# Kernel optimization log

Hardware: AMD Instinct MI355X
Metric: run time of the kernel (lower is better)

Reference implementation:

```python
import jax, jax.numpy as jnp
import numpy as np

B, NB, NV, H = 512, 3, 64, 256
CS = (40, 40)          # child branch lengths
COUP = (16, 48)        # parent vertices where child branches attach
IN = 9


def setup_inputs() -> dict:
    key = jax.random.key(0)
    ks = jax.random.split(key, 24)

    def w(k, shape, fan_in):
        return jax.random.uniform(k, shape, jnp.float32, -1.0, 1.0) / np.sqrt(fan_in)

    return {
        "current_vertices": jax.random.normal(ks[0], (B, NB, NV, 3), jnp.float32),
        "previous_vertices": jax.random.normal(ks[1], (B, NB, NV, 3), jnp.float32),
        "clamped_target_hints": jax.random.normal(ks[2], (B, NB, NV, 3), jnp.float32),
        # encoder
        "enc_w1": w(ks[3], (IN, H), IN), "enc_b1": w(ks[4], (H,), IN),
        "enc_w2": w(ks[5], (H, H), H), "enc_b2": w(ks[6], (H,), H),
        # child-sum tree-LSTM cell (bottom-up)
        "W_iou": w(ks[7], (H, 3 * H), H), "b_iou": w(ks[8], (3 * H,), H),
        "U_iou": w(ks[9], (H, 3 * H), H),
        "W_f": w(ks[10], (H, H), H), "b_f": w(ks[11], (H,), H),
        "U_f": w(ks[12], (H, H), H),
        # torch.nn.LSTMCell (top-down), gate order i,f,g,o
        "W_ih": w(ks[13], (H, 4 * H), H), "b_ih": w(ks[14], (4 * H,), H),
        "W_hh": w(ks[15], (H, 4 * H), H), "b_hh": w(ks[16], (4 * H,), H),
        # decoder
        "dec_w1": w(ks[17], (2 * H, H), 2 * H), "dec_b1": w(ks[18], (H,), 2 * H),
        "dec_w2": w(ks[19], (H, 3), H), "dec_b2": w(ks[20], (3,), H),
    }


def _forward(cv, pv, hints,
             enc_w1, enc_b1, enc_w2, enc_b2,
             W_iou, b_iou, U_iou, W_f, b_f, U_f,
             W_ih, b_ih, W_hh, b_hh,
             dec_w1, dec_b1, dec_w2, dec_b2):
    Bsz = cv.shape[0]
    nv = cv.shape[2]
    dt = cv.dtype
    feats = jnp.concatenate([cv, cv - pv, hints], axis=-1)            # [B,NB,NV,9]
    enc = jnp.maximum(feats @ enc_w1 + enc_b1, 0.0) @ enc_w2 + enc_b2  # [B,NB,NV,H]
    zero = jnp.zeros((Bsz, H), dt)

    # --- bottom-up: child-sum cell. A leaf with a single all-zero child is
    # mathematically identical to a zero initial carry (U_* have no bias),
    # so each chain is a plain scan from leaf toward vertex 0.
    def bu_chain_step(carry, x):
        h_prev, c_prev = carry
        iou = x @ W_iou + b_iou + h_prev @ U_iou
        i, o, u = jnp.split(iou, 3, axis=-1)
        f = jax.nn.sigmoid(x @ W_f + b_f + h_prev @ U_f)
        c = jax.nn.sigmoid(i) * jnp.tanh(u) + f * c_prev
        h = jax.nn.sigmoid(o) * jnp.tanh(c)
        return (h, c), (h, c)

    # child branches: leaf (v=L-1) -> v=0
    roots_h, roots_c, child_bu = [], [], []
    for k, L in enumerate(CS):
        xs = jnp.transpose(enc[:, k + 1, :L], (1, 0, 2))[::-1]  # time-major, reversed
        _, (hs, cs) = jax.lax.scan(bu_chain_step, (zero, zero), xs)
        hs, cs = hs[::-1], cs[::-1]                              # [L,B,H] indexed by v
        roots_h.append(hs[0]); roots_c.append(cs[0])
        child_bu.append((hs, cs))

    # coupled-child states injected at coupling vertices of the parent chain
    K = len(CS)
    coup_h = jnp.zeros((nv, K, Bsz, H), dt)
    coup_c = jnp.zeros_like(coup_h)
    coup_m = jnp.zeros((nv, K), dt)
    for k, ci in enumerate(COUP):
        coup_h = coup_h.at[ci, k].set(roots_h[k])
        coup_c = coup_c.at[ci, k].set(roots_c[k])
        coup_m = coup_m.at[ci, k].set(1.0)

    def bu_parent_step(carry, inp):
        h_prev, c_prev = carry
        x, ch, cc, m = inp  # ch,cc: [K,B,H]; m: [K]
        h_sum = h_prev + (m[:, None, None] * ch).sum(0)
        iou = x @ W_iou + b_iou + h_sum @ U_iou
        i, o, u = jnp.split(iou, 3, axis=-1)
        wf = x @ W_f + b_f
        fc = jax.nn.sigmoid(wf + h_prev @ U_f) * c_prev
        fc = fc + (m[:, None, None] * jax.nn.sigmoid(wf[None] + ch @ U_f) * cc).sum(0)
        c = jax.nn.sigmoid(i) * jnp.tanh(u) + fc
        h = jax.nn.sigmoid(o) * jnp.tanh(c)
        return (h, c), (h, c)

    xs0 = jnp.transpose(enc[:, 0], (1, 0, 2))  # [NV,B,H]
    _, (p_hs, p_cs) = jax.lax.scan(
        bu_parent_step, (zero, zero),
        (xs0[::-1], coup_h[::-1], coup_c[::-1], coup_m[::-1]))
    p_hs, p_cs = p_hs[::-1], p_cs[::-1]

    bu_h = jnp.zeros((Bsz, NB, nv, H), dt)
    bu_c = jnp.zeros_like(bu_h)
    bu_h = bu_h.at[:, 0].set(jnp.transpose(p_hs, (1, 0, 2)))
    bu_c = bu_c.at[:, 0].set(jnp.transpose(p_cs, (1, 0, 2)))
    for k, L in enumerate(CS):
        hs, cs = child_bu[k]
        bu_h = bu_h.at[:, k + 1, :L].set(jnp.transpose(hs, (1, 0, 2)))
        bu_c = bu_c.at[:, k + 1, :L].set(jnp.transpose(cs, (1, 0, 2)))

    # --- top-down: standard LSTMCell chains
    def td_step(carry, x):
        h, c = carry
        g = x @ W_ih + b_ih + h @ W_hh + b_hh
        i, f, gg, o = jnp.split(g, 4, axis=-1)
        c = jax.nn.sigmoid(f) * c + jax.nn.sigmoid(i) * jnp.tanh(gg)
        h = jax.nn.sigmoid(o) * jnp.tanh(c)
        return (h, c), (h, c)

    _, (t_hs, t_cs) = jax.lax.scan(td_step, (bu_h[:, 0, 0], bu_c[:, 0, 0]), xs0[1:])
    td_p_h = jnp.concatenate([bu_h[:, 0, 0][None], t_hs], 0)  # [NV,B,H]
    td_p_c = jnp.concatenate([bu_c[:, 0, 0][None], t_cs], 0)

    td_h = jnp.zeros_like(bu_h)
    td_h = td_h.at[:, 0].set(jnp.transpose(td_p_h, (1, 0, 2)))
    for k, L in enumerate(CS):
        xs = jnp.transpose(enc[:, k + 1, :L], (1, 0, 2))
        _, (hs, _) = jax.lax.scan(td_step, (td_p_h[COUP[k]], td_p_c[COUP[k]]), xs)
        td_h = td_h.at[:, k + 1, :L].set(jnp.transpose(hs, (1, 0, 2)))

    comb = jnp.concatenate([bu_h, td_h], axis=-1)  # [B,NB,NV,2H]
    delta = jnp.maximum(comb @ dec_w1 + dec_b1, 0.0) @ dec_w2 + dec_b2
    pred = cv + delta
    mask = jnp.ones((NB, nv, 1), dt)
    for k, L in enumerate(CS):
        mask = mask.at[k + 1, L:].set(0.0)
    return pred * mask[None]


def reference(current_vertices, previous_vertices, clamped_target_hints,
              enc_w1, enc_b1, enc_w2, enc_b2,
              W_iou, b_iou, U_iou, W_f, b_f, U_f,
              W_ih, b_ih, W_hh, b_hh,
              dec_w1, dec_b1, dec_w2, dec_b2):
    return _forward(current_vertices, previous_vertices, clamped_target_hints,
                    enc_w1, enc_b1, enc_w2, enc_b2,
                    W_iou, b_iou, U_iou, W_f, b_f, U_f,
                    W_ih, b_ih, W_hh, b_hh,
                    dec_w1, dec_b1, dec_w2, dec_b2)
```

## Files before the change

kernel.cpp:

```cpp
#include <hip/hip_runtime.h>
#include <hip/hip_bf16.h>
#include <hip/hip_fp8.h>


constexpr int Hd    = 256;
constexpr int NBv   = 3;
constexpr int NVv   = 64;
constexpr int BATCH = 512;
constexpr long long NROWS = (long long)BATCH * NBv * NVv;
constexpr int CLEN = 40;
constexpr int CI0 = 16, CI1 = 48;

typedef __hip_bfloat16 bf16;
typedef unsigned short ushort;
typedef unsigned char u8;
typedef __attribute__((ext_vector_type(8))) short short8;
typedef __attribute__((ext_vector_type(4))) float f32x4;
typedef __attribute__((ext_vector_type(2))) long longx2;

__device__ __forceinline__ float sigf(float x)   { return 1.f / (1.f + __expf(-x)); }
__device__ __forceinline__ float tanh_f(float x) { return 1.f - 2.f / (__expf(2.f * x) + 1.f); }

__device__ __forceinline__ ushort f2bf(float x) {
  unsigned u = __float_as_uint(x);
  return (ushort)((u + 0x7FFFu + ((u >> 16) & 1u)) >> 16);
}
__device__ __forceinline__ float bf2f(ushort u) {
  return __uint_as_float(((unsigned)u) << 16);
}
__device__ __forceinline__ u8 f2fp8(float x) {
  __hip_fp8_e4m3 q(x);
  return (u8)q.__x;
}


__global__ __launch_bounds__(256) void pack_bu8_kernel(
    const float* __restrict__ W_iou, const float* __restrict__ W_f,
    const float* __restrict__ U_iou, const float* __restrict__ U_f,
    u8* __restrict__ out)
{
  int u = blockIdx.x * 256 + threadIdx.x;
  int s = u & 1, l = (u >> 1) & 63, T = u >> 7;
  int kp = T & 7, nt = T >> 3;
  int ks = kp * 2 + s;
  int k0 = ks * 32 + (l >> 4) * 8;
  int n  = nt * 16 + (l & 15);
  unsigned long long r = 0;
#pragma unroll
  for (int j = 0; j < 8; ++j) {
    int k = k0 + j;
    float v;
    if (k < 256) v = (n < 768) ? W_iou[k * 768 + n] : W_f[k * 256 + (n - 768)];
    else         v = (n < 768) ? U_iou[(k - 256) * 768 + n] : U_f[(k - 256) * 256 + (n - 768)];
    r |= ((unsigned long long)f2fp8(v)) << (8 * j);
  }
  *(unsigned long long*)(out + (size_t)u * 8) = r;
}

__global__ __launch_bounds__(256) void pack_td8_kernel(
    const float* __restrict__ W_ih, const float* __restrict__ W_hh,
    u8* __restrict__ out)
{
  int u = blockIdx.x * 256 + threadIdx.x;
  int s = u & 1, l = (u >> 1) & 63, T = u >> 7;
  int kp = T & 7, nt = T >> 3;
  int ks = kp * 2 + s;
  int k0 = ks * 32 + (l >> 4) * 8;
  int n  = nt * 16 + (l & 15);
  unsigned long long r = 0;
#pragma unroll
  for (int j = 0; j < 8; ++j) {
    int k = k0 + j;
    float v = (k < 256) ? W_ih[k * 1024 + n] : W_hh[(k - 256) * 1024 + n];
    r |= ((unsigned long long)f2fp8(v)) << (8 * j);
  }
  *(unsigned long long*)(out + (size_t)u * 8) = r;
}

__global__ __launch_bounds__(256) void pack_wfx8_kernel(
    const float* __restrict__ W_f, u8* __restrict__ out)
{
  int u = blockIdx.x * 256 + threadIdx.x;
  int s = u & 1, l = (u >> 1) & 63, T = u >> 7;
  int kp = T & 3, nt = T >> 2;
  int ks = kp * 2 + s;
  int k0 = ks * 32 + (l >> 4) * 8;
  int n  = nt * 16 + (l & 15);
  unsigned long long r = 0;
#pragma unroll
  for (int j = 0; j < 8; ++j)
    r |= ((unsigned long long)f2fp8(W_f[(k0 + j) * 256 + n])) << (8 * j);
  *(unsigned long long*)(out + (size_t)u * 8) = r;
}

__global__ __launch_bounds__(256) void pack_encw2_kernel(
    const float* __restrict__ w2, ushort* __restrict__ out)
{
  int idx = blockIdx.x * 256 + threadIdx.x;
  int j = idx & 7, l = (idx >> 3) & 63, T = idx >> 9;
  int ks = T & 7, nt = T >> 3;
  int k = ks * 32 + (l >> 4) * 8 + j;
  int n = nt * 16 + (l & 15);
  out[idx] = f2bf(w2[k * 256 + n]);
}

__global__ __launch_bounds__(256) void pack_decw1_kernel(
    const float* __restrict__ w1, ushort* __restrict__ out)
{
  int idx = blockIdx.x * 256 + threadIdx.x;
  int j = idx & 7, l = (idx >> 3) & 63, T = idx >> 9;
  int ks = T & 15, nt = T >> 4;
  int k = ks * 32 + (l >> 4) * 8 + j;
  int n = nt * 16 + (l & 15);
  out[idx] = f2bf(w1[k * 256 + n]);
}

__global__ __launch_bounds__(256) void pack_decw2_kernel(
    const float* __restrict__ w2, ushort* __restrict__ out)
{
  int idx = blockIdx.x * 256 + threadIdx.x;
  int j = idx & 7, l = (idx >> 3) & 63, T = idx >> 9;
  int ks = T & 7;
  int k = ks * 32 + (l >> 4) * 8 + j;
  int n = l & 15;
  out[idx] = (n < 3) ? f2bf(w2[k * 3 + n]) : (ushort)0;
}

__device__ __forceinline__ short8 ldA16(const ushort* buf, int row, int kbyte) {
  int off = (row * 512 + kbyte) ^ ((row & 7) << 4);
  return *(const short8*)((const char*)buf + off);
}
__device__ __forceinline__ short8 ldA1024(const ushort* buf, int row, int kbyte) {
  int off = (row * 1024 + kbyte) ^ ((row & 7) << 4);
  return *(const short8*)((const char*)buf + off);
}
#define STA(BUF, R, JJ, BITS) { \
    int off_ = ((R) * 512 + (JJ) * 2) ^ (((R) & 7) << 4); \
    (BUF)[off_ >> 1] = (BITS); }
#define STA8(BUF, R, JJ, B8) { \
    int off_ = ((R) * 256 + (JJ)) ^ (((R) & 7) << 3); \
    (BUF)[off_] = (B8); }

__global__ __launch_bounds__(256) void enc_kernel(
    const float* __restrict__ cv, const float* __restrict__ pv,
    const float* __restrict__ hints,
    const float* __restrict__ w1, const float* __restrict__ b1,
    const ushort* __restrict__ w2p, const float* __restrict__ b2,
    ushort* __restrict__ enc)
{
  __shared__ float fs[32][10];
  __shared__ ushort h1L[32 * 256];
  const long long row0 = (long long)blockIdx.x * 32;
  const int tid = threadIdx.x;
  if (tid < 96) {
    int r = tid / 3, c = tid % 3;
    long long row = row0 + r;
    float a = cv[row * 3 + c];
    fs[r][c]     = a;
    fs[r][3 + c] = a - pv[row * 3 + c];
    fs[r][6 + c] = hints[row * 3 + c];
  }
  __syncthreads();
  {
    const int j = tid;
    float wc[9];
#pragma unroll
    for (int i = 0; i < 9; ++i) wc[i] = w1[i * 256 + j];
    const float bb = b1[j];
    for (int r = 0; r < 32; ++r) {
      float a = bb;
#pragma unroll
      for (int i = 0; i < 9; ++i) a += fs[r][i] * wc[i];
      ushort hb = f2bf(fmaxf(a, 0.f));
      STA(h1L, r, j, hb);
    }
  }
  __syncthreads();
  const int lane = tid & 63, w = tid >> 6;
  const int col = lane & 15, krow = lane >> 4, kb = krow * 16;
  const f32x4 zf4 = {0.f, 0.f, 0.f, 0.f};
  f32x4 acc[2][4];
#pragma unroll
  for (int m = 0; m < 2; ++m)
#pragma unroll
    for (int g = 0; g < 4; ++g) acc[m][g] = zf4;
#pragma unroll
  for (int ks = 0; ks < 8; ++ks) {
    short8 A[2];
#pragma unroll
    for (int m = 0; m < 2; ++m) A[m] = ldA16(h1L, m * 16 + col, ks * 64 + kb);
#pragma unroll
    for (int g = 0; g < 4; ++g) {
      short8 b = *(const short8*)(w2p + ((((w * 4 + g) * 8 + ks) * 64 + lane)) * 8);
#pragma unroll
      for (int m = 0; m < 2; ++m)
        acc[m][g] = __builtin_amdgcn_mfma_f32_16x16x32_bf16(A[m], b, acc[m][g], 0, 0, 0);
    }
  }
#pragma unroll
  for (int g = 0; g < 4; ++g) {
    const int jj = (w * 4 + g) * 16 + col;
    const float bb = b2[jj];
#pragma unroll
    for (int m = 0; m < 2; ++m)
#pragma unroll
      for (int q = 0; q < 4; ++q) {
        long long row = row0 + m * 16 + krow * 4 + q;
        enc[row * 256 + jj] = f2bf(acc[m][g][q] + bb);
      }
  }
}

template<int MT>
__device__ __forceinline__ void gemm_main8(
    const u8* __restrict__ W, const u8* __restrict__ AxL,
    const u8* __restrict__ AhL, f32x4 (&acc)[MT][4], int w, int lane)
{
  const int col = lane & 15;
  const int kb  = (lane >> 4) * 8;
  const int sw  = (col & 7) << 3;
#pragma unroll 4
  for (int kp = 0; kp < 8; ++kp) {
    const u8* Ab = (kp < 4) ? AxL : AhL;
    const int ksl = (kp & 3) * 2;
    long a[MT][2];
#pragma unroll
    for (int m = 0; m < MT; ++m) {
      int base = (m * 16 + col) * 256 + ksl * 32 + kb;
      a[m][0] = *(const long*)(Ab + ((base) ^ sw));
      a[m][1] = *(const long*)(Ab + ((base + 32) ^ sw));
    }
#pragma unroll
    for (int g = 0; g < 4; ++g) {
      longx2 bq = *(const longx2*)(W + ((size_t)(((g * 16 + w) * 8 + kp) * 64 + lane) << 4));
#pragma unroll
      for (int m = 0; m < MT; ++m) {
        acc[m][g] = __builtin_amdgcn_mfma_f32_16x16x32_fp8_fp8(a[m][0], bq[0], acc[m][g], 0, 0, 0);
        acc[m][g] = __builtin_amdgcn_mfma_f32_16x16x32_fp8_fp8(a[m][1], bq[1], acc[m][g], 0, 0, 0);
      }
    }
  }
}

__device__ __forceinline__ void gemm_side8(
    const u8* __restrict__ Wbu, const u8* __restrict__ Wfx,
    const u8* __restrict__ Rhb, const u8* __restrict__ AxL,
    f32x4 (&accs)[4], f32x4& accw, int w, int lane)
{
  const int col = lane & 15;
  const int kb  = (lane >> 4) * 8;
  const int sw  = (col & 7) << 3;
#pragma unroll
  for (int kp = 0; kp < 4; ++kp) {
    const int base = col * 256 + kp * 64 + kb;
    long ar0 = *(const long*)(Rhb + ((base) ^ sw));
    long ar1 = *(const long*)(Rhb + ((base + 32) ^ sw));
#pragma unroll
    for (int g = 0; g < 4; ++g) {
      longx2 bq = *(const longx2*)(Wbu + ((size_t)(((g * 16 + w) * 8 + kp + 4) * 64 + lane) << 4));
      accs[g] = __builtin_amdgcn_mfma_f32_16x16x32_fp8_fp8(ar0, bq[0], accs[g], 0, 0, 0);
      accs[g] = __builtin_amdgcn_mfma_f32_16x16x32_fp8_fp8(ar1, bq[1], accs[g], 0, 0, 0);
    }
    long ax0 = *(const long*)(AxL + ((base) ^ sw));
    long ax1 = *(const long*)(AxL + ((base + 32) ^ sw));
    longx2 bw = *(const longx2*)(Wfx + ((size_t)((w * 4 + kp) * 64 + lane) << 4));
    accw = __builtin_amdgcn_mfma_f32_16x16x32_fp8_fp8(ax0, bw[0], accw, 0, 0, 0);
    accw = __builtin_amdgcn_mfma_f32_16x16x32_fp8_fp8(ax1, bw[1], accw, 0, 0, 0);
  }
}

#define ZACC(MT_, A_) { \
  _Pragma("unroll") for (int m_ = 0; m_ < MT_; ++m_) \
  _Pragma("unroll") for (int g_ = 0; g_ < 4; ++g_) A_[m_][g_] = zf4; }

__global__ __launch_bounds__(1024, 4) void seq_kernel(
    const ushort* enc,
    const u8* __restrict__ Wbu, const u8* __restrict__ Wtd,
    const u8* __restrict__ Wfx,
    const float* __restrict__ b_iou, const float* __restrict__ b_f,
    const float* __restrict__ b_ih,  const float* __restrict__ b_hh,
    ushort* __restrict__ bu_h, ushort* td_h)
{
  __shared__ u8 Axb[2][32 * 256];
  __shared__ u8 Ahb[2][32 * 256];
  __shared__ u8 Rh[2][16 * 256];

  const int tid  = threadIdx.x;
  const int lane = tid & 63;
  const int w    = tid >> 6;
  const int b0   = blockIdx.x * 16;
  const int col  = lane & 15;
  const int krow = lane >> 4;
  const f32x4 zf4 = {0.f, 0.f, 0.f, 0.f};

  const int jj = w * 16 + col;
  const float bi0 = b_iou[jj], bi1 = b_iou[256 + jj], bi2 = b_iou[512 + jj];
  const float bfv = b_f[jj];
  const float bt0 = b_ih[jj]       + b_hh[jj];
  const float bt1 = b_ih[256 + jj] + b_hh[256 + jj];
  const float bt2 = b_ih[512 + jj] + b_hh[512 + jj];
  const float bt3 = b_ih[768 + jj] + b_hh[768 + jj];

  float c2[2][4];
  float rc0[4], rc1[4];
  float sc0[4], sc1[4];

#define SLOAD32(V, XV) { \
    int rr_ = tid >> 5, ch_ = tid & 31; \
    int mt_ = rr_ >> 4, br_ = rr_ & 15; \
    long long rowg_ = ((long long)(b0 + br_) * NBv + (mt_ + 1)) * NVv + (V); \
    XV = *(const short8*)(enc + rowg_ * 256 + ch_ * 8); }

#define SLOAD16(V, XV) if (tid < 512) { \
    int rr_ = tid >> 5, ch_ = tid & 31; \
    long long rowg_ = ((long long)(b0 + rr_) * NBv) * NVv + (V); \
    XV = *(const short8*)(enc + rowg_ * 256 + ch_ * 8); }

#define SWRITE(DST, XV, GUARD) if (GUARD) { \
    int rr_ = tid >> 5, ch_ = tid & 31; \
    unsigned long long r_ = 0; \
    _Pragma("unroll") for (int e_ = 0; e_ < 8; ++e_) \
      r_ |= ((unsigned long long)f2fp8(bf2f((ushort)XV[e_]))) << (8 * e_); \
    *(unsigned long long*)((DST) + (((rr_ * 256 + ch_ * 8) ^ ((rr_ & 7) << 3)))) = r_; }

  {
    *(unsigned long long*)(&Ahb[0][tid * 8]) = 0ull;
    short8 xv; SLOAD32(CLEN - 1, xv);
#pragma unroll
    for (int m = 0; m < 2; ++m)
#pragma unroll
      for (int q = 0; q < 4; ++q) c2[m][q] = 0.f;
    SWRITE(Axb[0], xv, true);
    __syncthreads();
    for (int s = 0; s < CLEN; ++s) {
      const int v = CLEN - 1 - s, pp = s & 1;
      short8 xn;
      if (s < CLEN - 1) SLOAD32(v - 1, xn);
      f32x4 acc[2][4]; ZACC(2, acc);
      gemm_main8<2>(Wbu, Axb[pp], Ahb[pp], acc, w, lane);
#pragma unroll
      for (int m = 0; m < 2; ++m)
#pragma unroll
        for (int q = 0; q < 4; ++q) {
          const int br = krow * 4 + q;
          float I = acc[m][0][q] + bi0;
          float O = acc[m][1][q] + bi1;
          float U = acc[m][2][q] + bi2;
          float F = acc[m][3][q] + bfv;
          float cn = sigf(I) * tanh_f(U) + sigf(F) * c2[m][q];
          float hn = sigf(O) * tanh_f(cn);
          c2[m][q] = cn;
          u8 hq = f2fp8(hn);
          STA8(Ahb[pp ^ 1], m * 16 + br, jj, hq);
          long long rowg = ((long long)(b0 + br) * NBv + (m + 1)) * NVv + v;
          bu_h[rowg * 256 + jj] = f2bf(hn);
          if (v == 0) {
            STA8(Rh[m], br, jj, hq);
            if (m == 0) rc0[q] = cn; else rc1[q] = cn;
          }
        }
      if (s < CLEN - 1) SWRITE(Axb[pp ^ 1], xn, true);
      __syncthreads();
    }
  }

  {
    if (tid < 512) *(unsigned long long*)(&Ahb[0][tid * 8]) = 0ull;
    short8 xv = {};
    SLOAD16(NVv - 1, xv);
#pragma unroll
    for (int q = 0; q < 4; ++q) c2[0][q] = 0.f;
    SWRITE(Axb[0], xv, (tid < 512));
    __syncthreads();
    for (int s = 0; s < NVv; ++s) {
      const int v = NVv - 1 - s, pp = s & 1;
      short8 xn = {};
      if (s < NVv - 1) SLOAD16(v - 1, xn);
      f32x4 acc[1][4]; ZACC(1, acc);
      gemm_main8<1>(Wbu, Axb[pp], Ahb[pp], acc, w, lane);
      const int ck = (v == CI0) ? 0 : ((v == CI1) ? 1 : -1);
      f32x4 accs[4]; f32x4 accw;
      if (ck >= 0) {
#pragma unroll
        for (int g = 0; g < 4; ++g) accs[g] = zf4;
        accw = zf4;
        const u8* Rp = (ck == 0) ? Rh[0] : Rh[1];
        gemm_side8(Wbu, Wfx, Rp, Axb[pp], accs, accw, w, lane);
      }
#pragma unroll
      for (int q = 0; q < 4; ++q) {
        const int br = krow * 4 + q;
        float I  = acc[0][0][q] + bi0;
        float O  = acc[0][1][q] + bi1;
        float U  = acc[0][2][q] + bi2;
        float F1 = acc[0][3][q] + bfv;
        float fc = sigf(F1) * c2[0][q];
        if (ck >= 0) {
          I += accs[0][q]; O += accs[1][q]; U += accs[2][q];
          float wfx = accw[q] + bfv;
          float rcv = (ck == 0) ? rc0[q] : rc1[q];
          fc += sigf(wfx + accs[3][q]) * rcv;
        }
        float cn = sigf(I) * tanh_f(U) + fc;
        float hn = sigf(O) * tanh_f(cn);
        c2[0][q] = cn;
        STA8(Ahb[pp ^ 1], br, jj, f2fp8(hn));
        long long rowg = ((long long)(b0 + br) * NBv) * NVv + v;
        bu_h[rowg * 256 + jj] = f2bf(hn);
        if (v == 0) td_h[rowg * 256 + jj] = f2bf(hn);
      }
      if (s < NVv - 1) SWRITE(Axb[pp ^ 1], xn, (tid < 512));
      __syncthreads();
    }
  }

  {
    short8 xv = {};
    SLOAD16(1, xv);
    SWRITE(Axb[0], xv, (tid < 512));
    __syncthreads();
    for (int s = 0; s < NVv - 1; ++s) {
      const int v = 1 + s, pp = s & 1;
      short8 xn = {};
      if (s < NVv - 2) SLOAD16(v + 1, xn);
      f32x4 acc[1][4]; ZACC(1, acc);
      gemm_main8<1>(Wtd, Axb[pp], Ahb[pp], acc, w, lane);
#pragma unroll
      for (int q = 0; q < 4; ++q) {
        const int br = krow * 4 + q;
        float I = acc[0][0][q] + bt0;
        float F = acc[0][1][q] + bt1;
        float G = acc[0][2][q] + bt2;
        float O = acc[0][3][q] + bt3;
        float cn = sigf(F) * c2[0][q] + sigf(I) * tanh_f(G);
        float hn = sigf(O) * tanh_f(cn);
        c2[0][q] = cn;
        u8 hq = f2fp8(hn);
        STA8(Ahb[pp ^ 1], br, jj, hq);
        long long rowg = ((long long)(b0 + br) * NBv) * NVv + v;
        td_h[rowg * 256 + jj] = f2bf(hn);
        if (v == CI0) { STA8(Rh[0], br, jj, hq); sc0[q] = cn; }
        if (v == CI1) { STA8(Rh[1], br, jj, hq); sc1[q] = cn; }
      }
      if (s < NVv - 2) SWRITE(Axb[pp ^ 1], xn, (tid < 512));
      __syncthreads();
    }
  }

  {
    {
      int rr = tid >> 5, ch = tid & 31;
      int mt = rr >> 4, br = rr & 15;
      unsigned long long vv = *(const unsigned long long*)(
          &Rh[mt][0] + (((br * 256 + ch * 8) ^ ((br & 7) << 3))));
      *(unsigned long long*)(&Ahb[0][0] + (((rr * 256 + ch * 8) ^ ((rr & 7) << 3)))) = vv;
    }
    short8 xv; SLOAD32(0, xv);
#pragma unroll
    for (int m = 0; m < 2; ++m)
#pragma unroll
      for (int q = 0; q < 4; ++q)
        c2[m][q] = (m == 0) ? sc0[q] : sc1[q];
    SWRITE(Axb[0], xv, true);
    __syncthreads();
    for (int s = 0; s < CLEN; ++s) {
      const int v = s, pp = s & 1;
      short8 xn;
      if (s < CLEN - 1) SLOAD32(v + 1, xn);
      f32x4 acc[2][4]; ZACC(2, acc);
      gemm_main8<2>(Wtd, Axb[pp], Ahb[pp], acc, w, lane);
#pragma unroll
      for (int m = 0; m < 2; ++m)
#pragma unroll
        for (int q = 0; q < 4; ++q) {
          const int br = krow * 4 + q;
          float I = acc[m][0][q] + bt0;
          float F = acc[m][1][q] + bt1;
          float G = acc[m][2][q] + bt2;
          float O = acc[m][3][q] + bt3;
          float cn = sigf(F) * c2[m][q] + sigf(I) * tanh_f(G);
          float hn = sigf(O) * tanh_f(cn);
          c2[m][q] = cn;
          STA8(Ahb[pp ^ 1], m * 16 + br, jj, f2fp8(hn));
          long long rowg = ((long long)(b0 + br) * NBv + (m + 1)) * NVv + v;
          td_h[rowg * 256 + jj] = f2bf(hn);
        }
      if (s < CLEN - 1) SWRITE(Axb[pp ^ 1], xn, true);
      __syncthreads();
    }
  }
}

__global__ __launch_bounds__(256) void dec_kernel(
    const ushort* __restrict__ bu_h, const ushort* __restrict__ td_h,
    const float* __restrict__ cv,
    const ushort* __restrict__ w1p, const float* __restrict__ b1,
    const ushort* __restrict__ w2p, const float* __restrict__ b2,
    float* __restrict__ out)
{
  __shared__ ushort combL[32 * 512];
  __shared__ ushort hidL[32 * 256];
  const long long row0 = (long long)blockIdx.x * 32;
  const int tid = threadIdx.x;

#pragma unroll
  for (int h = 0; h < 8; ++h) {
    int cid = tid + h * 256;
    int rr = cid >> 6, ch = cid & 63;
    long long row = row0 + rr;
    short8 v = (ch < 32)
        ? *(const short8*)(bu_h + row * 256 + ch * 8)
        : *(const short8*)(td_h + row * 256 + (ch - 32) * 8);
    *(short8*)((char*)combL + ((rr * 1024 + ch * 16) ^ ((rr & 7) << 4))) = v;
  }
  __syncthreads();

  const int lane = tid & 63, w = tid >> 6;
  const int col = lane & 15, krow = lane >> 4, kb = krow * 16;
  const f32x4 zf4 = {0.f, 0.f, 0.f, 0.f};
  f32x4 acc[2][4];
#pragma unroll
  for (int m = 0; m < 2; ++m)
#pragma unroll
    for (int g = 0; g < 4; ++g) acc[m][g] = zf4;
#pragma unroll 4
  for (int ks = 0; ks < 16; ++ks) {
    short8 A[2];
#pragma unroll
    for (int m = 0; m < 2; ++m) A[m] = ldA1024(combL, m * 16 + col, ks * 64 + kb);
#pragma unroll
    for (int g = 0; g < 4; ++g) {
      short8 b = *(const short8*)(w1p + ((((w * 4 + g) * 16 + ks) * 64 + lane)) * 8);
#pragma unroll
      for (int m = 0; m < 2; ++m)
        acc[m][g] = __builtin_amdgcn_mfma_f32_16x16x32_bf16(A[m], b, acc[m][g], 0, 0, 0);
    }
  }
#pragma unroll
  for (int g = 0; g < 4; ++g) {
    const int jj = (w * 4 + g) * 16 + col;
    const float bb = b1[jj];
#pragma unroll
    for (int m = 0; m < 2; ++m)
#pragma unroll
      for (int q = 0; q < 4; ++q) {
        ushort hb = f2bf(fmaxf(acc[m][g][q] + bb, 0.f));
        STA(hidL, m * 16 + krow * 4 + q, jj, hb);
      }
  }
  __syncthreads();

  if (w == 0) {
    f32x4 acc2[2]; acc2[0] = zf4; acc2[1] = zf4;
#pragma unroll
    for (int ks = 0; ks < 8; ++ks) {
      short8 bv = *(const short8*)(w2p + ((ks * 64 + lane)) * 8);
#pragma unroll
      for (int m = 0; m < 2; ++m) {
        short8 A = ldA16(hidL, m * 16 + col, ks * 64 + kb);
        acc2[m] = __builtin_amdgcn_mfma_f32_16x16x32_bf16(A, bv, acc2[m], 0, 0, 0);
      }
    }
    if (col < 3) {
      const float bb = b2[col];
#pragma unroll
      for (int m = 0; m < 2; ++m)
#pragma unroll
        for (int q = 0; q < 4; ++q) {
          long long row = row0 + m * 16 + krow * 4 + q;
          int v  = (int)(row & 63);
          int br = (int)((row >> 6) % 3);
          float res = 0.f;
          if (br == 0 || v < CLEN)
            res = cv[row * 3 + col] + acc2[m][q] + bb;
          out[row * 3 + col] = res;
        }
    }
  }
}

extern "C" void kernel_launch(void* const* d_in, const int* in_sizes, int n_in,
                              void* d_out, int out_size, void* d_ws, size_t ws_size,
                              hipStream_t stream) {
  const float* cv     = (const float*)d_in[0];
  const float* pv     = (const float*)d_in[1];
  const float* hints  = (const float*)d_in[2];
  const float* enc_w1 = (const float*)d_in[3];
  const float* enc_b1 = (const float*)d_in[4];
  const float* enc_w2 = (const float*)d_in[5];
  const float* enc_b2 = (const float*)d_in[6];
  const float* W_iou  = (const float*)d_in[7];
  const float* b_iou  = (const float*)d_in[8];
  const float* U_iou  = (const float*)d_in[9];
  const float* W_f    = (const float*)d_in[10];
  const float* b_f    = (const float*)d_in[11];
  const float* U_f    = (const float*)d_in[12];
  const float* W_ih   = (const float*)d_in[13];
  const float* b_ih   = (const float*)d_in[14];
  const float* W_hh   = (const float*)d_in[15];
  const float* b_hh   = (const float*)d_in[16];
  const float* dec_w1 = (const float*)d_in[17];
  const float* dec_b1 = (const float*)d_in[18];
  const float* dec_w2 = (const float*)d_in[19];
  const float* dec_b2 = (const float*)d_in[20];

  size_t act = (size_t)NROWS * 256;
  size_t need = 2 * act * 2
              + 2 * (size_t)524288 + 65536
              + (65536 + 131072 + 4096) * 2;
  if (ws_size < need) return;

  ushort* encW   = (ushort*)d_ws;
  ushort* buh    = encW + act;
  u8*     Wbu8   = (u8*)(buh + act);
  u8*     Wtd8   = Wbu8 + 524288;
  u8*     Wfx8   = Wtd8 + 524288;
  ushort* encw2p = (ushort*)(Wfx8 + 65536);
  ushort* decw1p = encw2p + 65536;
  ushort* decw2p = decw1p + 131072;

  pack_bu8_kernel<<<256, 256, 0, stream>>>(W_iou, W_f, U_iou, U_f, Wbu8);
  pack_td8_kernel<<<256, 256, 0, stream>>>(W_ih, W_hh, Wtd8);
  pack_wfx8_kernel<<<32, 256, 0, stream>>>(W_f, Wfx8);
  pack_encw2_kernel<<<256, 256, 0, stream>>>(enc_w2, encw2p);
  pack_decw1_kernel<<<512, 256, 0, stream>>>(dec_w1, decw1p);
  pack_decw2_kernel<<<16, 256, 0, stream>>>(dec_w2, decw2p);

  enc_kernel<<<(int)(NROWS / 32), 256, 0, stream>>>(cv, pv, hints, enc_w1, enc_b1,
                                                    encw2p, enc_b2, encW);
  seq_kernel<<<BATCH / 16, 1024, 0, stream>>>(encW, Wbu8, Wtd8, Wfx8, b_iou, b_f,
                                              b_ih, b_hh, buh, encW);
  dec_kernel<<<(int)(NROWS / 32), 256, 0, stream>>>(buh, encW, cv, decw1p, dec_b1,
                                                    decw2p, dec_b2, (float*)d_out);
}
```

Baseline: 1.936 ms.

## Keep half of recurrent weight fragments in registers and relayout fp8 LDS tiles

```diff
diff --git a/kernel.cpp b/kernel.cpp
--- a/kernel.cpp
+++ b/kernel.cpp
@@ -32,7 +32,19 @@
   __hip_fp8_e4m3 q(x);
   return (u8)q.__x;
 }
-
+template<bool HI>
+__device__ __forceinline__ unsigned cvtpk8(float a, float b, unsigned old) {
+#if __has_builtin(__builtin_amdgcn_cvt_pk_fp8_f32)
+  return (unsigned)__builtin_amdgcn_cvt_pk_fp8_f32(a, b, (int)old, HI);
+#else
+  __hip_fp8_e4m3 qa(a), qb(b);
+  unsigned v = (unsigned)qa.__x | ((unsigned)qb.__x << 8);
+  return HI ? ((old & 0xffffu) | (v << 16)) : ((old & 0xffff0000u) | v);
+#endif
+}
+__device__ __forceinline__ u8 f2fp8hw(float x) {
+  return (u8)(cvtpk8<false>(x, x, 0u) & 0xff);
+}
 
 __global__ __launch_bounds__(256) void pack_bu8_kernel(
     const float* __restrict__ W_iou, const float* __restrict__ W_f,
@@ -138,7 +150,8 @@
     int off_ = ((R) * 512 + (JJ) * 2) ^ (((R) & 7) << 4); \
     (BUF)[off_ >> 1] = (BITS); }
 #define STA8(BUF, R, JJ, B8) { \
-    int off_ = ((R) * 256 + (JJ)) ^ (((R) & 7) << 3); \
+    int p_ = ((JJ) >> 6) * 64 + (((JJ) >> 3) & 3) * 16 + (((JJ) >> 5) & 1) * 8 + ((JJ) & 7); \
+    int off_ = ((R) * 256 + p_) ^ (((R) & 7) << 4); \
     (BUF)[off_] = (B8); }
 
 __global__ __launch_bounds__(256) void enc_kernel(
@@ -214,24 +227,31 @@
 template<int MT>
 __device__ __forceinline__ void gemm_main8(
     const u8* __restrict__ W, const u8* __restrict__ AxL,
-    const u8* __restrict__ AhL, f32x4 (&acc)[MT][4], int w, int lane)
+    const u8* __restrict__ AhL, f32x4 (&acc)[MT][4],
+    const longx2 (&Bp0)[8], const longx2 (&Bp1)[8], int w, int lane)
 {
   const int col = lane & 15;
-  const int kb  = (lane >> 4) * 8;
-  const int sw  = (col & 7) << 3;
-#pragma unroll 4
+  const int grp = lane >> 4;
+  const int sw  = (col & 7) << 4;
+#pragma unroll
   for (int kp = 0; kp < 8; ++kp) {
     const u8* Ab = (kp < 4) ? AxL : AhL;
-    const int ksl = (kp & 3) * 2;
-    long a[MT][2];
+    const int kpl = kp & 3;
+    longx2 a[MT];
 #pragma unroll
     for (int m = 0; m < MT; ++m) {
-      int base = (m * 16 + col) * 256 + ksl * 32 + kb;
-      a[m][0] = *(const long*)(Ab + ((base) ^ sw));
-      a[m][1] = *(const long*)(Ab + ((base + 32) ^ sw));
-    }
-#pragma unroll
-    for (int g = 0; g < 4; ++g) {
+      int off = ((m * 16 + col) * 256 + kpl * 64 + grp * 16) ^ sw;
+      a[m] = *(const longx2*)(Ab + off);
+    }
+#pragma unroll
+    for (int m = 0; m < MT; ++m) {
+      acc[m][0] = __builtin_amdgcn_mfma_f32_16x16x32_fp8_fp8(a[m][0], Bp0[kp][0], acc[m][0], 0, 0, 0);
+      acc[m][0] = __builtin_amdgcn_mfma_f32_16x16x32_fp8_fp8(a[m][1], Bp0[kp][1], acc[m][0], 0, 0, 0);
+      acc[m][1] = __builtin_amdgcn_mfma_f32_16x16x32_fp8_fp8(a[m][0], Bp1[kp][0], acc[m][1], 0, 0, 0);
+      acc[m][1] = __builtin_amdgcn_mfma_f32_16x16x32_fp8_fp8(a[m][1], Bp1[kp][1], acc[m][1], 0, 0, 0);
+    }
+#pragma unroll
+    for (int g = 2; g < 4; ++g) {
       longx2 bq = *(const longx2*)(W + ((size_t)(((g * 16 + w) * 8 + kp) * 64 + lane) << 4));
 #pragma unroll
       for (int m = 0; m < MT; ++m) {
@@ -248,24 +268,22 @@
     f32x4 (&accs)[4], f32x4& accw, int w, int lane)
 {
   const int col = lane & 15;
-  const int kb  = (lane >> 4) * 8;
-  const int sw  = (col & 7) << 3;
+  const int grp = lane >> 4;
+  const int sw  = (col & 7) << 4;
 #pragma unroll
   for (int kp = 0; kp < 4; ++kp) {
-    const int base = col * 256 + kp * 64 + kb;
-    long ar0 = *(const long*)(Rhb + ((base) ^ sw));
-    long ar1 = *(const long*)(Rhb + ((base + 32) ^ sw));
+    const int base = (col * 256 + kp * 64 + grp * 16) ^ sw;
+    longx2 ar = *(const longx2*)(Rhb + base);
 #pragma unroll
     for (int g = 0; g < 4; ++g) {
       longx2 bq = *(const longx2*)(Wbu + ((size_t)(((g * 16 + w) * 8 + kp + 4) * 64 + lane) << 4));
-      accs[g] = __builtin_amdgcn_mfma_f32_16x16x32_fp8_fp8(ar0, bq[0], accs[g], 0, 0, 0);
-      accs[g] = __builtin_amdgcn_mfma_f32_16x16x32_fp8_fp8(ar1, bq[1], accs[g], 0, 0, 0);
-    }
-    long ax0 = *(const long*)(AxL + ((base) ^ sw));
-    long ax1 = *(const long*)(AxL + ((base + 32) ^ sw));
+      accs[g] = __builtin_amdgcn_mfma_f32_16x16x32_fp8_fp8(ar[0], bq[0], accs[g], 0, 0, 0);
+      accs[g] = __builtin_amdgcn_mfma_f32_16x16x32_fp8_fp8(ar[1], bq[1], accs[g], 0, 0, 0);
+    }
+    longx2 ax = *(const longx2*)(AxL + base);
     longx2 bw = *(const longx2*)(Wfx + ((size_t)((w * 4 + kp) * 64 + lane) << 4));
-    accw = __builtin_amdgcn_mfma_f32_16x16x32_fp8_fp8(ax0, bw[0], accw, 0, 0, 0);
-    accw = __builtin_amdgcn_mfma_f32_16x16x32_fp8_fp8(ax1, bw[1], accw, 0, 0, 0);
+    accw = __builtin_amdgcn_mfma_f32_16x16x32_fp8_fp8(ax[0], bw[0], accw, 0, 0, 0);
+    accw = __builtin_amdgcn_mfma_f32_16x16x32_fp8_fp8(ax[1], bw[1], accw, 0, 0, 0);
   }
 }
 
@@ -305,6 +323,12 @@
   float rc0[4], rc1[4];
   float sc0[4], sc1[4];
 
+  longx2 Bp0[8], Bp1[8];
+#define LOADBP(W_) { \
+    _Pragma("unroll") for (int kp_ = 0; kp_ < 8; ++kp_) { \
+      Bp0[kp_] = *(const longx2*)((W_) + ((size_t)((w * 8 + kp_) * 64 + lane) << 4)); \
+      Bp1[kp_] = *(const longx2*)((W_) + ((size_t)(((16 + w) * 8 + kp_) * 64 + lane) << 4)); } }
+
 #define SLOAD32(V, XV) { \
     int rr_ = tid >> 5, ch_ = tid & 31; \
     int mt_ = rr_ >> 4, br_ = rr_ & 15; \
@@ -318,12 +342,17 @@
 
 #define SWRITE(DST, XV, GUARD) if (GUARD) { \
     int rr_ = tid >> 5, ch_ = tid & 31; \
-    unsigned long long r_ = 0; \
-    _Pragma("unroll") for (int e_ = 0; e_ < 8; ++e_) \
-      r_ |= ((unsigned long long)f2fp8(bf2f((ushort)XV[e_]))) << (8 * e_); \
-    *(unsigned long long*)((DST) + (((rr_ * 256 + ch_ * 8) ^ ((rr_ & 7) << 3)))) = r_; }
+    unsigned w0_ = cvtpk8<false>(bf2f((ushort)XV[0]), bf2f((ushort)XV[1]), 0u); \
+    w0_ = cvtpk8<true>(bf2f((ushort)XV[2]), bf2f((ushort)XV[3]), w0_); \
+    unsigned w1_ = cvtpk8<false>(bf2f((ushort)XV[4]), bf2f((ushort)XV[5]), 0u); \
+    w1_ = cvtpk8<true>(bf2f((ushort)XV[6]), bf2f((ushort)XV[7]), w1_); \
+    int p0_ = (ch_ >> 3) * 64 + (ch_ & 3) * 16 + ((ch_ >> 2) & 1) * 8; \
+    int off_ = (rr_ * 256 + p0_) ^ ((rr_ & 7) << 4); \
+    unsigned long long r_ = (unsigned long long)w0_ | ((unsigned long long)w1_ << 32); \
+    *(unsigned long long*)((DST) + off_) = r_; }
 
   {
+    LOADBP(Wbu);
     *(unsigned long long*)(&Ahb[0][tid * 8]) = 0ull;
     short8 xv; SLOAD32(CLEN - 1, xv);
 #pragma unroll
@@ -337,7 +366,7 @@
       short8 xn;
       if (s < CLEN - 1) SLOAD32(v - 1, xn);
       f32x4 acc[2][4]; ZACC(2, acc);
-      gemm_main8<2>(Wbu, Axb[pp], Ahb[pp], acc, w, lane);
+      gemm_main8<2>(Wbu, Axb[pp], Ahb[pp], acc, Bp0, Bp1, w, lane);
 #pragma unroll
       for (int m = 0; m < 2; ++m)
 #pragma unroll
@@ -350,7 +379,7 @@
           float cn = sigf(I) * tanh_f(U) + sigf(F) * c2[m][q];
           float hn = sigf(O) * tanh_f(cn);
           c2[m][q] = cn;
-          u8 hq = f2fp8(hn);
+          u8 hq = f2fp8hw(hn);
           STA8(Ahb[pp ^ 1], m * 16 + br, jj, hq);
           long long rowg = ((long long)(b0 + br) * NBv + (m + 1)) * NVv + v;
           bu_h[rowg * 256 + jj] = f2bf(hn);
@@ -377,7 +406,7 @@
       short8 xn = {};
       if (s < NVv - 1) SLOAD16(v - 1, xn);
       f32x4 acc[1][4]; ZACC(1, acc);
-      gemm_main8<1>(Wbu, Axb[pp], Ahb[pp], acc, w, lane);
+      gemm_main8<1>(Wbu, Axb[pp], Ahb[pp], acc, Bp0, Bp1, w, lane);
       const int ck = (v == CI0) ? 0 : ((v == CI1) ? 1 : -1);
       f32x4 accs[4]; f32x4 accw;
       if (ck >= 0) {
@@ -404,7 +433,8 @@
         float cn = sigf(I) * tanh_f(U) + fc;
         float hn = sigf(O) * tanh_f(cn);
         c2[0][q] = cn;
-        STA8(Ahb[pp ^ 1], br, jj, f2fp8(hn));
+        u8 hq = f2fp8hw(hn);
+        STA8(Ahb[pp ^ 1], br, jj, hq);
         long long rowg = ((long long)(b0 + br) * NBv) * NVv + v;
         bu_h[rowg * 256 + jj] = f2bf(hn);
         if (v == 0) td_h[rowg * 256 + jj] = f2bf(hn);
@@ -415,6 +445,7 @@
   }
 
   {
+    LOADBP(Wtd);
     short8 xv = {};
     SLOAD16(1, xv);
     SWRITE(Axb[0], xv, (tid < 512));
@@ -424,7 +455,7 @@
       short8 xn = {};
       if (s < NVv - 2) SLOAD16(v + 1, xn);
       f32x4 acc[1][4]; ZACC(1, acc);
-      gemm_main8<1>(Wtd, Axb[pp], Ahb[pp], acc, w, lane);
+      gemm_main8<1>(Wtd, Axb[pp], Ahb[pp], acc, Bp0, Bp1, w, lane);
 #pragma unroll
       for (int q = 0; q < 4; ++q) {
         const int br = krow * 4 + q;
@@ -435,7 +466,7 @@
         float cn = sigf(F) * c2[0][q] + sigf(I) * tanh_f(G);
         float hn = sigf(O) * tanh_f(cn);
         c2[0][q] = cn;
-        u8 hq = f2fp8(hn);
+        u8 hq = f2fp8hw(hn);
         STA8(Ahb[pp ^ 1], br, jj, hq);
         long long rowg = ((long long)(b0 + br) * NBv) * NVv + v;
         td_h[rowg * 256 + jj] = f2bf(hn);
@@ -452,8 +483,8 @@
       int rr = tid >> 5, ch = tid & 31;
       int mt = rr >> 4, br = rr & 15;
       unsigned long long vv = *(const unsigned long long*)(
-          &Rh[mt][0] + (((br * 256 + ch * 8) ^ ((br & 7) << 3))));
-      *(unsigned long long*)(&Ahb[0][0] + (((rr * 256 + ch * 8) ^ ((rr & 7) << 3)))) = vv;
+          &Rh[mt][0] + (((br * 256 + ch * 8) ^ ((br & 7) << 4))));
+      *(unsigned long long*)(&Ahb[0][0] + (((rr * 256 + ch * 8) ^ ((rr & 7) << 4)))) = vv;
     }
     short8 xv; SLOAD32(0, xv);
 #pragma unroll
@@ -468,7 +499,7 @@
       short8 xn;
       if (s < CLEN - 1) SLOAD32(v + 1, xn);
       f32x4 acc[2][4]; ZACC(2, acc);
-      gemm_main8<2>(Wtd, Axb[pp], Ahb[pp], acc, w, lane);
+      gemm_main8<2>(Wtd, Axb[pp], Ahb[pp], acc, Bp0, Bp1, w, lane);
 #pragma unroll
       for (int m = 0; m < 2; ++m)
 #pragma unroll
@@ -481,7 +512,8 @@
           float cn = sigf(F) * c2[m][q] + sigf(I) * tanh_f(G);
           float hn = sigf(O) * tanh_f(cn);
           c2[m][q] = cn;
-          STA8(Ahb[pp ^ 1], m * 16 + br, jj, f2fp8(hn));
+          u8 hq = f2fp8hw(hn);
+          STA8(Ahb[pp ^ 1], m * 16 + br, jj, hq);
           long long rowg = ((long long)(b0 + br) * NBv + (m + 1)) * NVv + v;
           td_h[rowg * 256 + jj] = f2bf(hn);
         }
```

Result: slower. 2.572 ms (+32.8%).
